# Optimization experiments

Measured on AMD Instinct MI355X. Metric: run time of the kernel, lower is better.

## Reference

```python
import jax, jax.numpy as jnp
import numpy as np

B, C, T, H, W = 1, 512, 4, 32, 32
NUM_HEADS = 8
HEAD_DIM = C // NUM_HEADS


def setup_inputs() -> dict:
    key = jax.random.key(0)
    k1, k2, k3 = jax.random.split(key, 3)
    x = jax.random.normal(k1, (B, C, T, H, W), dtype=jnp.float32)
    w_qkv = jax.random.normal(k2, (3 * C, C), dtype=jnp.float32) * (1.0 / np.sqrt(C))
    w_out = jax.random.normal(k3, (C, C), dtype=jnp.float32) * (1.0 / np.sqrt(C))
    b_out = jnp.zeros((C,), dtype=jnp.float32)
    return {"x": x, "w_qkv": w_qkv, "w_out": w_out, "b_out": b_out}


def reference(x, w_qkv, w_out, b_out):
    b, c, t, h, w = x.shape
    n = t * h * w
    nh, hd = NUM_HEADS, c // NUM_HEADS
    x_flat = x.reshape(b, c, n)                      # [B,C,N]
    # 1x1 Conv3d == pointwise channel GEMM
    qkv = jnp.einsum('oc,bcn->bon', w_qkv, x_flat)   # [B,3C,N]
    q, k, v = jnp.split(qkv, 3, axis=1)
    q = q.reshape(b, nh, hd, n)
    k = k.reshape(b, nh, hd, n)
    v = v.reshape(b, nh, hd, n)
    dots = jnp.einsum('bhdi,bhdj->bhij', q, k) * (hd ** -0.5)  # [B,h,N,N]
    attn = jax.nn.softmax(dots, axis=-1)
    out = jnp.einsum('bhij,bhdj->bhdi', attn, v)     # [B,h,d,N]
    out = out.reshape(b, c, n)
    out = jnp.einsum('oc,bcn->bon', w_out, out) + b_out[None, :, None]
    return out.reshape(b, c, t, h, w) + x
```

## Files before the change

kernel.cpp:

```cpp
#include <hip/hip_runtime.h>
#include <hip/hip_bf16.h>


#define N_TOK 4096
#define C_DIM 512
#define NH    8
#define HD    64

#define QSCALE  0.18033688011112042f

typedef __bf16 bf16x8 __attribute__((ext_vector_type(8)));
typedef float f32x4 __attribute__((ext_vector_type(4)));

__device__ __forceinline__ f32x4 mfma16(bf16x8 a, bf16x8 b, f32x4 c) {
    return __builtin_amdgcn_mfma_f32_16x16x32_bf16(a, b, c, 0, 0, 0);
}

__device__ __forceinline__ bool probe_f32(const unsigned short* x) {
    int lane = threadIdx.x & 63;
    int hits = 0;
    #pragma unroll
    for (int r = 0; r < 4; r++) {
        unsigned short u = x[(lane * 4 + r) * 2];
        hits += (((u >> 7) & 0xFF) >= 140) ? 1 : 0;
    }
    #pragma unroll
    for (int off = 1; off < 64; off <<= 1) hits += __shfl_xor(hits, off);
    return hits >= 8;
}

__global__ __launch_bounds__(256) void prepare(
    const void* __restrict__ xv, const void* __restrict__ wq,
    const void* __restrict__ wo, const void* __restrict__ bo,
    __hip_bfloat16* __restrict__ xt, __hip_bfloat16* __restrict__ wqc,
    __hip_bfloat16* __restrict__ woc, __hip_bfloat16* __restrict__ bc)
{
    bool f32 = probe_f32((const unsigned short*)xv);
    int b = blockIdx.x, tid = threadIdx.x;
    if (b < 512) {
        __shared__ __hip_bfloat16 t[64][68];
        int n0 = (b & 63) * 64, c0 = (b >> 6) * 64;
        int nl = tid & 15, cl = tid >> 4;
        #pragma unroll
        for (int p = 0; p < 4; p++) {
            int c = cl + p * 16;
            ushort4 pk;
            if (f32) {
                float4 v = *reinterpret_cast<const float4*>(
                    (const float*)xv + (size_t)(c0 + c) * N_TOK + n0 + nl * 4);
                union { unsigned short u; __hip_bfloat16 h; } a0, a1, a2, a3;
                a0.h = __float2bfloat16(v.x); a1.h = __float2bfloat16(v.y);
                a2.h = __float2bfloat16(v.z); a3.h = __float2bfloat16(v.w);
                pk.x = a0.u; pk.y = a1.u; pk.z = a2.u; pk.w = a3.u;
            } else {
                pk = *reinterpret_cast<const ushort4*>(
                    (const __hip_bfloat16*)xv + (size_t)(c0 + c) * N_TOK + n0 + nl * 4);
            }
            *reinterpret_cast<ushort4*>(&t[c][nl * 4]) = pk;
        }
        __syncthreads();
        int cc = tid & 15, nr = tid >> 4;
        #pragma unroll
        for (int p = 0; p < 4; p++) {
            int n = nr + p * 16;
            ushort4 v;
            v.x = *reinterpret_cast<unsigned short*>(&t[cc * 4 + 0][n]);
            v.y = *reinterpret_cast<unsigned short*>(&t[cc * 4 + 1][n]);
            v.z = *reinterpret_cast<unsigned short*>(&t[cc * 4 + 2][n]);
            v.w = *reinterpret_cast<unsigned short*>(&t[cc * 4 + 3][n]);
            *reinterpret_cast<ushort4*>(xt + (size_t)(n0 + n) * C_DIM + c0 + cc * 4) = v;
        }
    } else {
        const int N1 = 3 * C_DIM * C_DIM, N2 = C_DIM * C_DIM, N3 = C_DIM;
        int total4 = (N1 + N2 + N3) >> 2;
        int stride = 128 * 256;
        for (int g = (b - 512) * 256 + tid; g < total4; g += stride) {
            int i = g * 4;
            const void* src; __hip_bfloat16* dst; int j;
            if (i < N1)           { src = wq; dst = wqc; j = i; }
            else if (i < N1 + N2) { src = wo; dst = woc; j = i - N1; }
            else                  { src = bo; dst = bc;  j = i - N1 - N2; }
            ushort4 pk;
            if (f32) {
                float4 v = *reinterpret_cast<const float4*>((const float*)src + j);
                union { unsigned short u; __hip_bfloat16 h; } a0, a1, a2, a3;
                a0.h = __float2bfloat16(v.x); a1.h = __float2bfloat16(v.y);
                a2.h = __float2bfloat16(v.z); a3.h = __float2bfloat16(v.w);
                pk.x = a0.u; pk.y = a1.u; pk.z = a2.u; pk.w = a3.u;
            } else {
                pk = *reinterpret_cast<const ushort4*>((const __hip_bfloat16*)src + j);
            }
            *reinterpret_cast<ushort4*>(dst + j) = pk;
        }
    }
}

__global__ __launch_bounds__(128) void qkv_gemm(
    const __hip_bfloat16* __restrict__ w,
    const __hip_bfloat16* __restrict__ xt,
    __hip_bfloat16* __restrict__ qt,
    unsigned char* __restrict__ kvg)
{
    __shared__ alignas(16) unsigned char sx[2][16384];
    __shared__ alignas(16) unsigned char swt[2][8192];
    int tid = threadIdx.x, lane = tid & 63, wv = tid >> 6;
    int l15 = lane & 15, quad = lane >> 4;
    int n0b = blockIdx.x * 128;
    int n0w = n0b + wv * 64;
    int m0w = blockIdx.y * 64;
    int rl = lane >> 3, cs = lane & 7;

    f32x4 acc[4][4] = {};

    auto stageF = [&](int c, int buf) {
        #pragma unroll
        for (int k = 0; k < 8; k++) {
            int g = wv * 8 + k;
            int row = g * 8 + rl;
            const unsigned char* src = (const unsigned char*)xt
                + (size_t)(n0b + row) * 1024 + c * 128 + ((cs ^ (row & 7)) << 4);
            __builtin_amdgcn_global_load_lds(
                (const __attribute__((address_space(1))) void*)src,
                (__attribute__((address_space(3))) void*)(&sx[buf][g * 1024]),
                16, 0, 0);
        }
        #pragma unroll
        for (int k = 0; k < 4; k++) {
            int g = wv * 4 + k;
            int row = g * 8 + rl;
            const unsigned char* src = (const unsigned char*)w
                + (size_t)(m0w + row) * 1024 + c * 128 + ((cs ^ (row & 7)) << 4);
            __builtin_amdgcn_global_load_lds(
                (const __attribute__((address_space(1))) void*)src,
                (__attribute__((address_space(3))) void*)(&swt[buf][g * 1024]),
                16, 0, 0);
        }
    };

    auto compute = [&](int buf) {
        bf16x8 af[2][4], bfr[2][4];
        #pragma unroll
        for (int hf = 0; hf < 2; hf++) {
            #pragma unroll
            for (int i = 0; i < 4; i++) {
                int row = wv * 64 + i * 16 + l15;
                af[hf][i] = *reinterpret_cast<const bf16x8*>(
                    &sx[buf][row * 128 + (((hf * 4 + quad) ^ (row & 7)) << 4)]);
            }
            #pragma unroll
            for (int j = 0; j < 4; j++) {
                int row = j * 16 + l15;
                bfr[hf][j] = *reinterpret_cast<const bf16x8*>(
                    &swt[buf][row * 128 + (((hf * 4 + quad) ^ (row & 7)) << 4)]);
            }
        }
        #pragma unroll
        for (int hf = 0; hf < 2; hf++)
            #pragma unroll
            for (int i = 0; i < 4; i++)
                #pragma unroll
                for (int j = 0; j < 4; j++)
                    acc[i][j] = mfma16(af[hf][i], bfr[hf][j], acc[i][j]);
    };

    stageF(0, 0);
    #pragma unroll
    for (int c = 0; c < 8; c++) {
        if (c + 1 < 8) stageF(c + 1, (c + 1) & 1);
        if (c + 1 < 8) asm volatile("s_waitcnt vmcnt(12)" ::: "memory");
        else           asm volatile("s_waitcnt vmcnt(0)" ::: "memory");
        __builtin_amdgcn_s_barrier();
        __builtin_amdgcn_sched_barrier(0);
        compute(c & 1);
        asm volatile("" ::: "memory");
        __builtin_amdgcn_s_barrier();
    }

    int kind = m0w >> 9;
    int h = (m0w >> 6) & 7;
    int jb = n0w >> 6;
    unsigned char* sb = &sx[0][wv * 8192];
    #pragma unroll
    for (int i = 0; i < 4; i++)
        #pragma unroll
        for (int j = 0; j < 4; j++)
            #pragma unroll
            for (int r = 0; r < 4; r++) {
                int nn = i * 16 + quad * 4 + r;
                int dd = j * 16 + l15;
                float v = acc[i][j][r];
                int row, cg, byo;
                if (kind == 0)      { row = nn; cg = dd >> 3;              byo = (dd & 7) * 2; v *= QSCALE; }
                else if (kind == 1) { row = nn; cg = (dd >> 3) ^ (nn & 7); byo = (dd & 7) * 2; }
                else {
                    row = dd;
                    int cc = ((nn >> 5) << 2) | ((nn >> 2) & 3);
                    cg = cc ^ (dd & 7);
                    byo = ((nn >> 4) & 1) * 8 + (nn & 3) * 2;
                }
                int phys = cg ^ ((row >> 1) & 7);
                *reinterpret_cast<__hip_bfloat16*>(sb + row * 128 + phys * 16 + byo)
                    = __float2bfloat16(v);
            }
    unsigned char* gbase;
    if (kind == 0) gbase = (unsigned char*)(qt + ((size_t)h * N_TOK + n0w) * HD);
    else           gbase = kvg + (((size_t)h * 64 + jb) << 14) + (kind == 2 ? 8192 : 0);
    #pragma unroll
    for (int it = 0; it < 8; it++) {
        int idx = it * 64 + lane;
        int row = idx >> 3, phys = (idx & 7) ^ ((idx >> 4) & 7);
        uint4 val = *reinterpret_cast<const uint4*>(sb + row * 128 + phys * 16);
        *reinterpret_cast<uint4*>(gbase + idx * 16) = val;
    }
}

__global__ __launch_bounds__(256) void attn_kernel(
    const __hip_bfloat16* __restrict__ qt,
    const unsigned char* __restrict__ kv,
    __hip_bfloat16* __restrict__ Opart,
    float* __restrict__ lpart,
    __hip_bfloat16* __restrict__ ot,
    int tbase, int trem)
{
    __shared__ alignas(16) unsigned char kvb[4][16384];
    int tid = threadIdx.x, lane = tid & 63, wv = tid >> 6;
    int l15 = lane & 15, quad = lane >> 4;
    int s7 = l15 & 7;
    int h = blockIdx.x >> 4;
    int i0 = (blockIdx.x & 15) * 256 + wv * 64;
    int kslice = blockIdx.y;
    const unsigned char* kvh = kv + ((size_t)h << 20);

    int jt0 = kslice * tbase + min(kslice, trem);
    int ntile = tbase + (kslice < trem ? 1 : 0);

    bf16x8 qB[4][2];
    #pragma unroll
    for (int g = 0; g < 4; g++)
        #pragma unroll
        for (int hf = 0; hf < 2; hf++)
            qB[g][hf] = *reinterpret_cast<const bf16x8*>(
                qt + (h * N_TOK + i0 + g * 16 + l15) * HD + hf * 32 + quad * 8);

    bf16x8 vones;
    #pragma unroll
    for (int i = 0; i < 8; i++) vones[i] = (__bf16)1.0f;

    f32x4 oacc[4][4] = {};
    f32x4 lsum[4] = {};

    int koff[2], vo[2];
    #pragma unroll
    for (int hf = 0; hf < 2; hf++)
        koff[hf] = l15 * 128 + (((hf * 4 + quad) ^ s7) << 4);
    #pragma unroll
    for (int p = 0; p < 2; p++)
        vo[p] = l15 * 128 + (((p * 4 + quad) ^ s7) << 4);

    auto stage = [&](int jb, int buf) {
        const unsigned char* s = kvh + ((size_t)jb << 14) + wv * 4096 + lane * 16;
        unsigned char* d = &kvb[buf][0] + wv * 4096;
        #pragma unroll
        for (int it = 0; it < 4; it++)
            __builtin_amdgcn_global_load_lds(
                (const __attribute__((address_space(1))) void*)(s + it * 1024),
                (__attribute__((address_space(3))) void*)(d + it * 1024),
                16, 0, 0);
    };

    auto body = [&](const unsigned char* kb) {
        const unsigned char* vb = kb + 8192;
        bf16x8 kf[8];
        #pragma unroll
        for (int nt = 0; nt < 4; nt++)
            #pragma unroll
            for (int hf = 0; hf < 2; hf++)
                kf[nt * 2 + hf] = *reinterpret_cast<const bf16x8*>(kb + nt * 2048 + koff[hf]);
        bf16x8 vf[4][2];
        #pragma unroll
        for (int db = 0; db < 4; db++)
            #pragma unroll
            for (int p = 0; p < 2; p++)
                vf[db][p] = *reinterpret_cast<const bf16x8*>(vb + db * 2048 + vo[p]);

        f32x4 sA[4], sB[4];
        #pragma unroll
        for (int nt = 0; nt < 4; nt++) {
            f32x4 z = {};
            z = mfma16(kf[nt * 2], qB[0][0], z);
            sA[nt] = mfma16(kf[nt * 2 + 1], qB[0][1], z);
        }
        #pragma unroll
        for (int g = 0; g < 4; g++) {
            f32x4* scur = (g & 1) ? sB : sA;
            f32x4* snxt = (g & 1) ? sA : sB;
            if (g < 3) {
                #pragma unroll
                for (int nt = 0; nt < 4; nt++) {
                    f32x4 z = {};
                    z = mfma16(kf[nt * 2], qB[g + 1][0], z);
                    snxt[nt] = mfma16(kf[nt * 2 + 1], qB[g + 1][1], z);
                }
            }
            bf16x8 pf[2];
            #pragma unroll
            for (int p = 0; p < 2; p++)
                #pragma unroll
                for (int i = 0; i < 4; i++) {
                    pf[p][i]     = (__bf16)__builtin_amdgcn_exp2f(scur[p * 2][i]);
                    pf[p][i + 4] = (__bf16)__builtin_amdgcn_exp2f(scur[p * 2 + 1][i]);
                }
            #pragma unroll
            for (int p = 0; p < 2; p++) {
                #pragma unroll
                for (int db = 0; db < 4; db++)
                    oacc[g][db] = mfma16(pf[p], vf[db][p], oacc[g][db]);
                lsum[g] = mfma16(pf[p], vones, lsum[g]);
            }
        }
    };

    stage(jt0, 0);
    if (ntile > 1) stage(jt0 + 1, 1);
    if (ntile > 2) stage(jt0 + 2, 2);
    for (int t = 0; t < ntile; t++) {
        if (t + 2 < ntile)      asm volatile("s_waitcnt vmcnt(8)" ::: "memory");
        else if (t + 1 < ntile) asm volatile("s_waitcnt vmcnt(4)" ::: "memory");
        else                    asm volatile("s_waitcnt vmcnt(0)" ::: "memory");
        __builtin_amdgcn_s_barrier();
        __builtin_amdgcn_sched_barrier(0);
        if (t + 3 < ntile) stage(jt0 + t + 3, (t + 3) & 3);
        body(&kvb[t & 3][0]);
    }

    if (Opart) {
        __hip_bfloat16* Ob = Opart + (size_t)kslice * (NH * N_TOK * HD);
        float* lb = lpart + (size_t)kslice * (NH * N_TOK);
        #pragma unroll
        for (int g = 0; g < 4; g++) {
            #pragma unroll
            for (int db = 0; db < 4; db++)
                #pragma unroll
                for (int r = 0; r < 4; r++) {
                    int i = i0 + g * 16 + quad * 4 + r;
                    Ob[(h * N_TOK + i) * HD + db * 16 + l15] =
                        __float2bfloat16(oacc[g][db][r]);
                }
            if (l15 == 0)
                #pragma unroll
                for (int r = 0; r < 4; r++)
                    lb[h * N_TOK + i0 + g * 16 + quad * 4 + r] = lsum[g][r];
        }
    } else {
        #pragma unroll
        for (int g = 0; g < 4; g++)
            #pragma unroll
            for (int db = 0; db < 4; db++)
                #pragma unroll
                for (int r = 0; r < 4; r++) {
                    int i = i0 + g * 16 + quad * 4 + r;
                    ot[i * C_DIM + h * HD + db * 16 + l15] =
                        __float2bfloat16(oacc[g][db][r] / lsum[g][r]);
                }
    }
}

__global__ __launch_bounds__(256) void combine_kernel(
    const __hip_bfloat16* __restrict__ Opart, const float* __restrict__ lpart,
    __hip_bfloat16* __restrict__ ot, int splitk)
{
    int tid = blockIdx.x * 256 + threadIdx.x;
    int h = tid >> 16, rem = tid & 65535;
    int q = rem >> 4, d4 = rem & 15;
    size_t off = ((size_t)(h * N_TOK + q) * HD) + d4 * 4;
    float o[4] = {};
    float l = 0.f;
    for (int k = 0; k < splitk; k++) {
        ushort4 u = *reinterpret_cast<const ushort4*>(
            Opart + (size_t)k * (NH * N_TOK * HD) + off);
        union { unsigned short us; __hip_bfloat16 h; } c0, c1, c2, c3;
        c0.us = u.x; c1.us = u.y; c2.us = u.z; c3.us = u.w;
        o[0] += __bfloat162float(c0.h); o[1] += __bfloat162float(c1.h);
        o[2] += __bfloat162float(c2.h); o[3] += __bfloat162float(c3.h);
        l += lpart[k * (NH * N_TOK) + h * N_TOK + q];
    }
    float inv = 1.0f / l;
    union { unsigned long long u; __hip_bfloat16 b[4]; } pk;
    #pragma unroll
    for (int i = 0; i < 4; i++) pk.b[i] = __float2bfloat16(o[i] * inv);
    *reinterpret_cast<unsigned long long*>(ot + q * C_DIM + h * HD + d4 * 4) = pk.u;
}

__global__ __launch_bounds__(256) void proj_gemm(
    const __hip_bfloat16* __restrict__ w,
    const __hip_bfloat16* __restrict__ ot,
    const __hip_bfloat16* __restrict__ bias,
    const void* __restrict__ xv,
    void* __restrict__ outv)
{
    __shared__ alignas(16) unsigned char sot[2][16384];
    __shared__ alignas(16) unsigned char swt[2][4096];
    bool f32 = probe_f32((const unsigned short*)xv);
    int tid = threadIdx.x, lane = tid & 63, wv = tid >> 6;
    int l15 = lane & 15, quad = lane >> 4;
    int m0 = blockIdx.y * 32;
    int n0b = blockIdx.x * 128;
    int n0 = n0b + wv * 32;
    int rl = lane >> 3, cs = lane & 7;

    f32x4 acc[2][2] = {};

    auto stageF = [&](int c, int buf) {
        #pragma unroll
        for (int k = 0; k < 4; k++) {
            int g = wv * 4 + k;
            int row = g * 8 + rl;
            const unsigned char* src = (const unsigned char*)ot
                + (size_t)(n0b + row) * 1024 + c * 128 + ((cs ^ (row & 7)) << 4);
            __builtin_amdgcn_global_load_lds(
                (const __attribute__((address_space(1))) void*)src,
                (__attribute__((address_space(3))) void*)(&sot[buf][g * 1024]),
                16, 0, 0);
        }
        {
            int g = wv;
            int row = g * 8 + rl;
            const unsigned char* src = (const unsigned char*)w
                + (size_t)(m0 + row) * 1024 + c * 128 + ((cs ^ (row & 7)) << 4);
            __builtin_amdgcn_global_load_lds(
                (const __attribute__((address_space(1))) void*)src,
                (__attribute__((address_space(3))) void*)(&swt[buf][g * 1024]),
                16, 0, 0);
        }
    };

    auto compute = [&](int buf) {
        bf16x8 af[2][2], bfr[2][2];
        #pragma unroll
        for (int hf = 0; hf < 2; hf++) {
            #pragma unroll
            for (int mt = 0; mt < 2; mt++) {
                int row = mt * 16 + l15;
                af[hf][mt] = *reinterpret_cast<const bf16x8*>(
                    &swt[buf][row * 128 + (((hf * 4 + quad) ^ (row & 7)) << 4)]);
            }
            #pragma unroll
            for (int nt = 0; nt < 2; nt++) {
                int row = wv * 32 + nt * 16 + l15;
                bfr[hf][nt] = *reinterpret_cast<const bf16x8*>(
                    &sot[buf][row * 128 + (((hf * 4 + quad) ^ (row & 7)) << 4)]);
            }
        }
        #pragma unroll
        for (int hf = 0; hf < 2; hf++)
            #pragma unroll
            for (int mt = 0; mt < 2; mt++)
                #pragma unroll
                for (int nt = 0; nt < 2; nt++)
                    acc[mt][nt] = mfma16(af[hf][mt], bfr[hf][nt], acc[mt][nt]);
    };

    stageF(0, 0);
    #pragma unroll
    for (int c = 0; c < 8; c++) {
        if (c + 1 < 8) stageF(c + 1, (c + 1) & 1);
        if (c + 1 < 8) asm volatile("s_waitcnt vmcnt(5)" ::: "memory");
        else           asm volatile("s_waitcnt vmcnt(0)" ::: "memory");
        __builtin_amdgcn_s_barrier();
        __builtin_amdgcn_sched_barrier(0);
        compute(c & 1);
        asm volatile("" ::: "memory");
        __builtin_amdgcn_s_barrier();
    }

    #pragma unroll
    for (int mt = 0; mt < 2; mt++)
        #pragma unroll
        for (int nt = 0; nt < 2; nt++)
            #pragma unroll
            for (int r = 0; r < 4; r++) {
                int m = m0 + mt * 16 + quad * 4 + r;
                int n = n0 + nt * 16 + l15;
                int idx = m * N_TOK + n;
                float xr = f32 ? ((const float*)xv)[idx]
                               : __bfloat162float(((const __hip_bfloat16*)xv)[idx]);
                float v = acc[mt][nt][r] + __bfloat162float(bias[m]) + xr;
                if (f32) ((float*)outv)[idx] = v;
                else     ((__hip_bfloat16*)outv)[idx] = __float2bfloat16(v);
            }
}

extern "C" void kernel_launch(void* const* d_in, const int* in_sizes, int n_in,
                              void* d_out, int out_size, void* d_ws, size_t ws_size,
                              hipStream_t stream) {
    const void* x     = d_in[0];
    const void* w_qkv = d_in[1];
    const void* w_out = d_in[2];
    const void* b_out = d_in[3];

    char* ws = (char*)d_ws;
    const size_t MB = 1024 * 1024;
    __hip_bfloat16* xt  = (__hip_bfloat16*)(ws);
    __hip_bfloat16* ot  = (__hip_bfloat16*)(ws);
    __hip_bfloat16* qt  = (__hip_bfloat16*)(ws + 4 * MB);
    unsigned char*  kv  = (unsigned char*) (ws + 8 * MB);
    __hip_bfloat16* wqc = (__hip_bfloat16*)(ws + 16 * MB);
    __hip_bfloat16* woc = (__hip_bfloat16*)(ws + 16 * MB + 0x180000);
    __hip_bfloat16* bc  = (__hip_bfloat16*)(ws + 16 * MB + 0x200000);

    const size_t pbase   = 16 * MB + 0x200800;
    const size_t o_slice = (size_t)NH * N_TOK * HD * 2;
    const size_t l_slice = (size_t)NH * N_TOK * 4;
    int nslice = 1;
    if      (ws_size >= pbase + 4 * (o_slice + l_slice)) nslice = 4;
    else if (ws_size >= pbase + 3 * (o_slice + l_slice)) nslice = 3;
    else if (ws_size >= pbase + 2 * (o_slice + l_slice)) nslice = 2;
    __hip_bfloat16* Opart = (nslice > 1) ? (__hip_bfloat16*)(ws + pbase) : nullptr;
    float* lpart = (nslice > 1) ? (float*)(ws + pbase + (size_t)nslice * o_slice) : nullptr;

    prepare<<<640, 256, 0, stream>>>(x, w_qkv, w_out, b_out, xt, wqc, woc, bc);
    qkv_gemm<<<dim3(32, 24), 128, 0, stream>>>(wqc, xt, qt, kv);

    int tbase = 64 / nslice, trem = 64 % nslice;
    attn_kernel<<<dim3(128, nslice), 256, 0, stream>>>(
        qt, kv, Opart, lpart, ot, tbase, trem);
    if (nslice > 1)
        combine_kernel<<<2048, 256, 0, stream>>>(Opart, lpart, ot, nslice);

    proj_gemm<<<dim3(32, 16), 256, 0, stream>>>(woc, ot, bc, x, d_out);
}
```

Baseline: 136.0 us.

## Fuse split-K attention combine into output projection GEMM

When the attention runs with four key slices, the separate combine kernel is removed and its work moves into the projection GEMM. Each block reads the partial O slices and row sums, normalises them into bf16 in shared memory, and feeds them straight to the MFMA loop. The whole W_out tile is preloaded into LDS. This saves a kernel launch and the round trip of the combined output through global memory. In exchange, each of the 16 m-blocks re-reads and re-reduces the same partial slices, and the fused path loses the asynchronous double-buffered pipelining of the old loop.

After: 158.2 us. 16.3% more time.

```diff
diff --git a/kernel.cpp b/kernel.cpp
--- a/kernel.cpp
+++ b/kernel.cpp
@@ -14,6 +14,10 @@
 
 __device__ __forceinline__ f32x4 mfma16(bf16x8 a, bf16x8 b, f32x4 c) {
     return __builtin_amdgcn_mfma_f32_16x16x32_bf16(a, b, c, 0, 0, 0);
+}
+
+__device__ __forceinline__ float bfu(unsigned int u16) {
+    union { unsigned int i; float f; } t; t.i = u16 << 16; return t.f;
 }
 
 __device__ __forceinline__ bool probe_f32(const unsigned short* x) {
@@ -396,10 +400,12 @@
     const __hip_bfloat16* __restrict__ ot,
     const __hip_bfloat16* __restrict__ bias,
     const void* __restrict__ xv,
-    void* __restrict__ outv)
+    void* __restrict__ outv,
+    const __hip_bfloat16* __restrict__ Opart,
+    const float* __restrict__ lpart)
 {
     __shared__ alignas(16) unsigned char sot[2][16384];
-    __shared__ alignas(16) unsigned char swt[2][4096];
+    __shared__ alignas(16) unsigned char sw[32768];
     bool f32 = probe_f32((const unsigned short*)xv);
     int tid = threadIdx.x, lane = tid & 63, wv = tid >> 6;
     int l15 = lane & 15, quad = lane >> 4;
@@ -410,67 +416,149 @@
 
     f32x4 acc[2][2] = {};
 
-    auto stageF = [&](int c, int buf) {
-        #pragma unroll
-        for (int k = 0; k < 4; k++) {
-            int g = wv * 4 + k;
-            int row = g * 8 + rl;
-            const unsigned char* src = (const unsigned char*)ot
-                + (size_t)(n0b + row) * 1024 + c * 128 + ((cs ^ (row & 7)) << 4);
-            __builtin_amdgcn_global_load_lds(
-                (const __attribute__((address_space(1))) void*)src,
-                (__attribute__((address_space(3))) void*)(&sot[buf][g * 1024]),
-                16, 0, 0);
-        }
-        {
-            int g = wv;
-            int row = g * 8 + rl;
-            const unsigned char* src = (const unsigned char*)w
-                + (size_t)(m0 + row) * 1024 + c * 128 + ((cs ^ (row & 7)) << 4);
-            __builtin_amdgcn_global_load_lds(
-                (const __attribute__((address_space(1))) void*)src,
-                (__attribute__((address_space(3))) void*)(&swt[buf][g * 1024]),
-                16, 0, 0);
-        }
-    };
-
-    auto compute = [&](int buf) {
-        bf16x8 af[2][2], bfr[2][2];
-        #pragma unroll
-        for (int hf = 0; hf < 2; hf++) {
-            #pragma unroll
-            for (int mt = 0; mt < 2; mt++) {
-                int row = mt * 16 + l15;
-                af[hf][mt] = *reinterpret_cast<const bf16x8*>(
-                    &swt[buf][row * 128 + (((hf * 4 + quad) ^ (row & 7)) << 4)]);
-            }
-            #pragma unroll
-            for (int nt = 0; nt < 2; nt++) {
-                int row = wv * 32 + nt * 16 + l15;
-                bfr[hf][nt] = *reinterpret_cast<const bf16x8*>(
-                    &sot[buf][row * 128 + (((hf * 4 + quad) ^ (row & 7)) << 4)]);
-            }
-        }
-        #pragma unroll
-        for (int hf = 0; hf < 2; hf++)
-            #pragma unroll
-            for (int mt = 0; mt < 2; mt++)
-                #pragma unroll
-                for (int nt = 0; nt < 2; nt++)
-                    acc[mt][nt] = mfma16(af[hf][mt], bfr[hf][nt], acc[mt][nt]);
-    };
-
-    stageF(0, 0);
-    #pragma unroll
-    for (int c = 0; c < 8; c++) {
-        if (c + 1 < 8) stageF(c + 1, (c + 1) & 1);
-        if (c + 1 < 8) asm volatile("s_waitcnt vmcnt(5)" ::: "memory");
-        else           asm volatile("s_waitcnt vmcnt(0)" ::: "memory");
-        __builtin_amdgcn_s_barrier();
-        __builtin_amdgcn_sched_barrier(0);
-        compute(c & 1);
-        asm volatile("" ::: "memory");
-        __builtin_amdgcn_s_barrier();
+    if (Opart) {
+        #pragma unroll
+        for (int c2 = 0; c2 < 2; c2++) {
+            int c = wv * 2 + c2;
+            #pragma unroll
+            for (int k = 0; k < 4; k++) {
+                int row = k * 8 + rl;
+                const unsigned char* src = (const unsigned char*)w
+                    + (size_t)(m0 + row) * 1024 + c * 128 + ((cs ^ (row & 7)) << 4);
+                __builtin_amdgcn_global_load_lds(
+                    (const __attribute__((address_space(1))) void*)src,
+                    (__attribute__((address_space(3))) void*)(&sw[c * 4096 + k * 1024]),
+                    16, 0, 0);
+            }
+        }
+        int row = tid >> 1;
+        int s0 = (tid & 1) * 4;
+        int r7 = row & 7;
+        int n = n0b + row;
+        #pragma unroll
+        for (int c = 0; c < 8; c++) {
+            uint4 ld[16];
+            float lv[4];
+            #pragma unroll
+            for (int j = 0; j < 4; j++) {
+                int segl = (s0 + j) ^ r7;
+                #pragma unroll
+                for (int k = 0; k < 4; k++)
+                    ld[j * 4 + k] = *reinterpret_cast<const uint4*>(
+                        Opart + ((size_t)k * (NH * N_TOK) + c * N_TOK + n) * HD + segl * 8);
+            }
+            #pragma unroll
+            for (int k = 0; k < 4; k++)
+                lv[k] = lpart[k * (NH * N_TOK) + c * N_TOK + n];
+            float inv = 1.0f / (lv[0] + lv[1] + lv[2] + lv[3]);
+            auto fold = [&](unsigned int d0, unsigned int d1,
+                            unsigned int d2, unsigned int d3) -> unsigned int {
+                float a0 = bfu(d0 & 0xffffu) + bfu(d1 & 0xffffu)
+                         + bfu(d2 & 0xffffu) + bfu(d3 & 0xffffu);
+                float a1 = bfu(d0 >> 16) + bfu(d1 >> 16)
+                         + bfu(d2 >> 16) + bfu(d3 >> 16);
+                union { unsigned short us; __hip_bfloat16 h; } p0, p1;
+                p0.h = __float2bfloat16(a0 * inv);
+                p1.h = __float2bfloat16(a1 * inv);
+                return (unsigned int)p0.us | ((unsigned int)p1.us << 16);
+            };
+            #pragma unroll
+            for (int j = 0; j < 4; j++) {
+                uint4 o4;
+                o4.x = fold(ld[j*4+0].x, ld[j*4+1].x, ld[j*4+2].x, ld[j*4+3].x);
+                o4.y = fold(ld[j*4+0].y, ld[j*4+1].y, ld[j*4+2].y, ld[j*4+3].y);
+                o4.z = fold(ld[j*4+0].z, ld[j*4+1].z, ld[j*4+2].z, ld[j*4+3].z);
+                o4.w = fold(ld[j*4+0].w, ld[j*4+1].w, ld[j*4+2].w, ld[j*4+3].w);
+                *reinterpret_cast<uint4*>(&sot[c & 1][row * 128 + (s0 + j) * 16]) = o4;
+            }
+            __syncthreads();
+            {
+                bf16x8 af[2][2], bfr[2][2];
+                #pragma unroll
+                for (int hf = 0; hf < 2; hf++) {
+                    #pragma unroll
+                    for (int mt = 0; mt < 2; mt++) {
+                        int rw = mt * 16 + l15;
+                        af[hf][mt] = *reinterpret_cast<const bf16x8*>(
+                            &sw[c * 4096 + rw * 128 + (((hf * 4 + quad) ^ (rw & 7)) << 4)]);
+                    }
+                    #pragma unroll
+                    for (int nt = 0; nt < 2; nt++) {
+                        int rw = wv * 32 + nt * 16 + l15;
+                        bfr[hf][nt] = *reinterpret_cast<const bf16x8*>(
+                            &sot[c & 1][rw * 128 + (((hf * 4 + quad) ^ (rw & 7)) << 4)]);
+                    }
+                }
+                #pragma unroll
+                for (int hf = 0; hf < 2; hf++)
+                    #pragma unroll
+                    for (int mt = 0; mt < 2; mt++)
+                        #pragma unroll
+                        for (int nt = 0; nt < 2; nt++)
+                            acc[mt][nt] = mfma16(af[hf][mt], bfr[hf][nt], acc[mt][nt]);
+            }
+        }
+    } else {
+        unsigned char (*swb)[4096] = reinterpret_cast<unsigned char(*)[4096]>(sw);
+        auto stageF = [&](int c, int buf) {
+            #pragma unroll
+            for (int k = 0; k < 4; k++) {
+                int g = wv * 4 + k;
+                int row = g * 8 + rl;
+                const unsigned char* src = (const unsigned char*)ot
+                    + (size_t)(n0b + row) * 1024 + c * 128 + ((cs ^ (row & 7)) << 4);
+                __builtin_amdgcn_global_load_lds(
+                    (const __attribute__((address_space(1))) void*)src,
+                    (__attribute__((address_space(3))) void*)(&sot[buf][g * 1024]),
+                    16, 0, 0);
+            }
+            {
+                int row = wv * 8 + rl;
+                const unsigned char* src = (const unsigned char*)w
+                    + (size_t)(m0 + row) * 1024 + c * 128 + ((cs ^ (row & 7)) << 4);
+                __builtin_amdgcn_global_load_lds(
+                    (const __attribute__((address_space(1))) void*)src,
+                    (__attribute__((address_space(3))) void*)(&swb[buf][wv * 1024]),
+                    16, 0, 0);
+            }
+        };
+        auto computeO = [&](int buf) {
+            bf16x8 af[2][2], bfr[2][2];
+            #pragma unroll
+            for (int hf = 0; hf < 2; hf++) {
+                #pragma unroll
+                for (int mt = 0; mt < 2; mt++) {
+                    int row = mt * 16 + l15;
+                    af[hf][mt] = *reinterpret_cast<const bf16x8*>(
+                        &swb[buf][row * 128 + (((hf * 4 + quad) ^ (row & 7)) << 4)]);
+                }
+                #pragma unroll
+                for (int nt = 0; nt < 2; nt++) {
+                    int row = wv * 32 + nt * 16 + l15;
+                    bfr[hf][nt] = *reinterpret_cast<const bf16x8*>(
+                        &sot[buf][row * 128 + (((hf * 4 + quad) ^ (row & 7)) << 4)]);
+                }
+            }
+            #pragma unroll
+            for (int hf = 0; hf < 2; hf++)
+                #pragma unroll
+                for (int mt = 0; mt < 2; mt++)
+                    #pragma unroll
+                    for (int nt = 0; nt < 2; nt++)
+                        acc[mt][nt] = mfma16(af[hf][mt], bfr[hf][nt], acc[mt][nt]);
+        };
+        stageF(0, 0);
+        #pragma unroll
+        for (int c = 0; c < 8; c++) {
+            if (c + 1 < 8) stageF(c + 1, (c + 1) & 1);
+            if (c + 1 < 8) asm volatile("s_waitcnt vmcnt(5)" ::: "memory");
+            else           asm volatile("s_waitcnt vmcnt(0)" ::: "memory");
+            __builtin_amdgcn_s_barrier();
+            __builtin_amdgcn_sched_barrier(0);
+            computeO(c & 1);
+            asm volatile("" ::: "memory");
+            __builtin_amdgcn_s_barrier();
+        }
     }
 
     #pragma unroll
@@ -480,8 +568,8 @@
             #pragma unroll
             for (int r = 0; r < 4; r++) {
                 int m = m0 + mt * 16 + quad * 4 + r;
-                int n = n0 + nt * 16 + l15;
-                int idx = m * N_TOK + n;
+                int nn = n0 + nt * 16 + l15;
+                int idx = m * N_TOK + nn;
                 float xr = f32 ? ((const float*)xv)[idx]
                                : __bfloat162float(((const __hip_bfloat16*)xv)[idx]);
                 float v = acc[mt][nt][r] + __bfloat162float(bias[m]) + xr;
@@ -524,8 +612,14 @@
     int tbase = 64 / nslice, trem = 64 % nslice;
     attn_kernel<<<dim3(128, nslice), 256, 0, stream>>>(
         qt, kv, Opart, lpart, ot, tbase, trem);
-    if (nslice > 1)
-        combine_kernel<<<2048, 256, 0, stream>>>(Opart, lpart, ot, nslice);
-
-    proj_gemm<<<dim3(32, 16), 256, 0, stream>>>(woc, ot, bc, x, d_out);
-}
+
+    if (nslice == 4) {
+        proj_gemm<<<dim3(32, 16), 256, 0, stream>>>(
+            woc, ot, bc, x, d_out, Opart, lpart);
+    } else {
+        if (nslice > 1)
+            combine_kernel<<<2048, 256, 0, stream>>>(Opart, lpart, ot, nslice);
+        proj_gemm<<<dim3(32, 16), 256, 0, stream>>>(
+            woc, ot, bc, x, d_out, nullptr, nullptr);
+    }
+}
```
